# Kernel optimization log

Hardware: AMD Instinct MI355X
Metric: run time of the kernel (lower is better)

## Reference

```python
import jax, jax.numpy as jnp
import numpy as np


def setup_inputs() -> dict:
    key = jax.random.key(0)
    k1, k2, k3 = jax.random.split(key, 3)
    B, H, D, N = 2, 16, 64, 2048
    return {
        "query": jax.random.normal(k1, (B, H, D, N), dtype=jnp.float32),
        "key": jax.random.normal(k2, (B, H, D, N), dtype=jnp.float32),
        "value": jax.random.normal(k3, (B, H, D, N), dtype=jnp.float32),
    }


def reference(query, key, value):
    # NOTE: original torch code scales by sqrt(query.size(-1)) which,
    # given the [B,H,d,N] layout, is sqrt(N) (the sequence length), not sqrt(d).
    scale = query.shape[-1] ** 0.5
    # scores[b,h,q,k] = sum_d query[b,h,d,q] * key[b,h,d,k]
    scores = jnp.einsum("bhdq,bhdk->bhqk", query, key) / scale
    attn = jax.nn.softmax(scores, axis=-1)
    # out[b,h,q,v] = sum_k attn[b,h,q,k] * value[b,h,v,k]
    return jnp.einsum("bhqk,bhvk->bhqv", attn, value)
```

## Files before the change

### kernel.cpp

```cpp
#include <hip/hip_runtime.h>
#include <hip/hip_bf16.h>


typedef __attribute__((ext_vector_type(8))) short short8;
typedef __attribute__((ext_vector_type(4))) float f32x4;

#define NN 2048
#define DD 64

#if __has_builtin(__builtin_amdgcn_exp2f)
#define EXP2(x) __builtin_amdgcn_exp2f(x)
#else
#define EXP2(x) __expf(0.69314718056f * (x))
#endif

__device__ __forceinline__ unsigned pk2(float a, float b) {
  __hip_bfloat162 h = __float22bfloat162_rn(make_float2(a, b));
  unsigned u; __builtin_memcpy(&u, &h, 4); return u;
}
__device__ __forceinline__ short f2bf(float f) {
  union { float f; unsigned u; } x; x.f = f;
  unsigned r = (x.u + 0x7fffu + ((x.u >> 16) & 1u)) >> 16;
  return (short)r;
}

__global__ __launch_bounds__(256, 2) void attn_kernel(
    const float* __restrict__ Q, const float* __restrict__ K,
    const float* __restrict__ V, float* __restrict__ Out) {
  const int tid  = threadIdx.x;
  const int wave = tid >> 6, lane = tid & 63;
  const int quad = lane >> 4, l16 = lane & 15;
  const int sw   = l16 & 7;

  const int bh   = blockIdx.x >> 4;
  const int qblk = blockIdx.x & 15;

  const float* Qh = Q + (size_t)bh * DD * NN;
  const float* Kh = K + (size_t)bh * DD * NN;
  const float* Vh = V + (size_t)bh * DD * NN;
  float*       Oh = Out + (size_t)bh * NN * DD;

  __shared__ __align__(16) char ldsK[2][64 * 128];
  __shared__ __align__(16) char ldsV[2][64 * 128];
  __shared__ __align__(16) char ldsP[8][16 * 128];

  const float qscale = 0.031881407f;
  short8 bQ[2][2];
  int qb[2];
#pragma unroll
  for (int qt = 0; qt < 2; ++qt) {
    qb[qt] = qblk * 128 + (wave * 2 + qt) * 16;
#pragma unroll
    for (int h = 0; h < 2; ++h)
#pragma unroll
      for (int j = 0; j < 8; ++j) {
        int d = h * 32 + quad * 8 + j;
        bQ[qt][h][j] = f2bf(Qh[(size_t)d * NN + qb[qt] + l16] * qscale);
      }
  }

  f32x4 accO[2][4];
#pragma unroll
  for (int qt = 0; qt < 2; ++qt)
#pragma unroll
    for (int vt = 0; vt < 4; ++vt) accO[qt][vt] = (f32x4){0.f, 0.f, 0.f, 0.f};
  float lp[2] = {0.f, 0.f};

  const int da = tid & 15;
  const int kb4 = (tid >> 4) * 4;
  const int vv = tid >> 2;
  const int vko = (tid & 3) * 16;
  const float* kbase = Kh + (size_t)(da * 4) * NN + kb4;
  const float* vbase = Vh + (size_t)vv * NN + vko;
  char* Pq0 = ldsP[wave * 2];
  char* Pq1 = ldsP[wave * 2 + 1];

  float kreg[4][4];
  float4 vf0, vf1, vf2, vf3;
  auto load_kv = [&](int k0) {
#pragma unroll
    for (int i = 0; i < 4; ++i) {
      float4 t = *(const float4*)(kbase + (size_t)i * NN + k0);
      kreg[i][0] = t.x; kreg[i][1] = t.y; kreg[i][2] = t.z; kreg[i][3] = t.w;
    }
    const float4* pv = (const float4*)(vbase + k0);
    vf0 = pv[0]; vf1 = pv[1]; vf2 = pv[2]; vf3 = pv[3];
  };
  auto store_kv = [&](char* bK, char* bV) {
#pragma unroll
    for (int j = 0; j < 4; ++j) {
      int key = kb4 + j;
      int phys = (da >> 1) ^ (key & 7);
      uint2 w; w.x = pk2(kreg[0][j], kreg[1][j]); w.y = pk2(kreg[2][j], kreg[3][j]);
      *(uint2*)&bK[key * 128 + phys * 16 + (da & 1) * 8] = w;
    }
    int ph0 = ((vko >> 3)) ^ (vv & 7);
    int ph1 = ((vko >> 3) + 1) ^ (vv & 7);
    uint4 w0 = make_uint4(pk2(vf0.x, vf0.y), pk2(vf0.z, vf0.w),
                          pk2(vf1.x, vf1.y), pk2(vf1.z, vf1.w));
    uint4 w1 = make_uint4(pk2(vf2.x, vf2.y), pk2(vf2.z, vf2.w),
                          pk2(vf3.x, vf3.y), pk2(vf3.z, vf3.w));
    *(uint4*)&bV[vv * 128 + ph0 * 16] = w0;
    *(uint4*)&bV[vv * 128 + ph1 * 16] = w1;
  };

  load_kv(0);
  store_kv(ldsK[0], ldsV[0]);
  __syncthreads();

#pragma unroll 2
  for (int it = 0; it < 32; ++it) {
    const int cur = it & 1;
    load_kv(((it + 1) & 31) * 64);

    const char* cK = ldsK[cur];
    const char* cV = ldsV[cur];

    f32x4 s[2][4];
#pragma unroll
    for (int kt = 0; kt < 4; ++kt) {
      const int key = kt * 16 + l16;
      short8 aK0 = *(const short8*)&cK[key * 128 + ((quad)     ^ sw) * 16];
      short8 aK1 = *(const short8*)&cK[key * 128 + ((quad + 4) ^ sw) * 16];
      f32x4 z = (f32x4){0.f, 0.f, 0.f, 0.f};
      s[0][kt] = __builtin_amdgcn_mfma_f32_16x16x32_bf16(aK0, bQ[0][0], z, 0, 0, 0);
      s[0][kt] = __builtin_amdgcn_mfma_f32_16x16x32_bf16(aK1, bQ[0][1], s[0][kt], 0, 0, 0);
      s[1][kt] = __builtin_amdgcn_mfma_f32_16x16x32_bf16(aK0, bQ[1][0], z, 0, 0, 0);
      s[1][kt] = __builtin_amdgcn_mfma_f32_16x16x32_bf16(aK1, bQ[1][1], s[1][kt], 0, 0, 0);
    }

#pragma unroll
    for (int qt = 0; qt < 2; ++qt) {
      char* Pq = qt ? Pq1 : Pq0;
#pragma unroll
      for (int kt = 0; kt < 4; ++kt) {
        float p0 = EXP2(s[qt][kt][0]);
        float p1 = EXP2(s[qt][kt][1]);
        float p2 = EXP2(s[qt][kt][2]);
        float p3 = EXP2(s[qt][kt][3]);
        lp[qt] += (p0 + p1) + (p2 + p3);
        uint2 w; w.x = pk2(p0, p1); w.y = pk2(p2, p3);
        int phys = ((kt << 1) | (quad >> 1)) ^ sw;
        *(uint2*)&Pq[l16 * 128 + phys * 16 + (quad & 1) * 8] = w;
      }
    }

#pragma unroll
    for (int h2 = 0; h2 < 2; ++h2) {
      const int pg = (h2 * 4 + quad) ^ sw;
      short8 aP0 = *(const short8*)&Pq0[l16 * 128 + pg * 16];
      short8 aP1 = *(const short8*)&Pq1[l16 * 128 + pg * 16];
#pragma unroll
      for (int vt = 0; vt < 4; ++vt) {
        short8 bV = *(const short8*)&cV[(vt * 16 + l16) * 128 + pg * 16];
        accO[0][vt] = __builtin_amdgcn_mfma_f32_16x16x32_bf16(aP0, bV, accO[0][vt], 0, 0, 0);
        accO[1][vt] = __builtin_amdgcn_mfma_f32_16x16x32_bf16(aP1, bV, accO[1][vt], 0, 0, 0);
      }
    }

    store_kv(ldsK[cur ^ 1], ldsV[cur ^ 1]);
    __syncthreads();
  }

#pragma unroll
  for (int qt = 0; qt < 2; ++qt) {
    float l = lp[qt];
    l += __shfl_xor(l, 16, 64);
    l += __shfl_xor(l, 32, 64);
#pragma unroll
    for (int r = 0; r < 4; ++r) {
      float lr  = __shfl(l, quad * 4 + r, 64);
      float inv = 1.0f / lr;
      int q = qb[qt] + quad * 4 + r;
#pragma unroll
      for (int vt = 0; vt < 4; ++vt)
        Oh[(size_t)q * DD + vt * 16 + l16] = accO[qt][vt][r] * inv;
    }
  }
}

extern "C" void kernel_launch(void* const* d_in, const int* in_sizes, int n_in,
                              void* d_out, int out_size, void* d_ws, size_t ws_size,
                              hipStream_t stream) {
  const float* Q = (const float*)d_in[0];
  const float* K = (const float*)d_in[1];
  const float* V = (const float*)d_in[2];
  float* O = (float*)d_out;
  dim3 grid(2 * 16 * (NN / 128));
  attn_kernel<<<grid, dim3(256), 0, stream>>>(Q, K, V, O);
}
```

Measured before the change: 149.1 us.

## Halve queries per block, double grid, and map heads to XCDs

Each wave now handles one 16-query tile instead of two, so a block covers 64 queries and the grid doubles to 1024 blocks. Launch bounds allow 4 blocks per CU, and block indices are remapped so all blocks of a head land on the same XCD, aiming for better L2 reuse of K and V. The cost is that each block re-reads and converts the full K/V stream for half as much compute, doubling global K/V traffic and LDS staging work per query. It also drops the unroll pragma on the main loop.

After: 174.6 us. +17.1%, slower.

```diff
diff --git a/kernel.cpp b/kernel.cpp
--- a/kernel.cpp
+++ b/kernel.cpp
@@ -24,7 +24,7 @@
   return (short)r;
 }
 
-__global__ __launch_bounds__(256, 2) void attn_kernel(
+__global__ __launch_bounds__(256, 4) void attn_kernel(
     const float* __restrict__ Q, const float* __restrict__ K,
     const float* __restrict__ V, float* __restrict__ Out) {
   const int tid  = threadIdx.x;
@@ -32,8 +32,9 @@
   const int quad = lane >> 4, l16 = lane & 15;
   const int sw   = l16 & 7;
 
-  const int bh   = blockIdx.x >> 4;
-  const int qblk = blockIdx.x & 15;
+  const int xcd  = blockIdx.x & 7, slot = blockIdx.x >> 3;
+  const int bh   = xcd * 4 + (slot >> 5);
+  const int qblk = slot & 31;
 
   const float* Qh = Q + (size_t)bh * DD * NN;
   const float* Kh = K + (size_t)bh * DD * NN;
@@ -42,38 +43,31 @@
 
   __shared__ __align__(16) char ldsK[2][64 * 128];
   __shared__ __align__(16) char ldsV[2][64 * 128];
-  __shared__ __align__(16) char ldsP[8][16 * 128];
+  __shared__ __align__(16) char ldsP[4][16 * 128];
 
   const float qscale = 0.031881407f;
-  short8 bQ[2][2];
-  int qb[2];
+  const int q0 = qblk * 64 + wave * 16;
+  short8 bQ[2];
 #pragma unroll
-  for (int qt = 0; qt < 2; ++qt) {
-    qb[qt] = qblk * 128 + (wave * 2 + qt) * 16;
+  for (int h = 0; h < 2; ++h)
 #pragma unroll
-    for (int h = 0; h < 2; ++h)
+    for (int j = 0; j < 8; ++j) {
+      int d = h * 32 + quad * 8 + j;
+      bQ[h][j] = f2bf(Qh[(size_t)d * NN + q0 + l16] * qscale);
+    }
+
+  f32x4 accO[4];
 #pragma unroll
-      for (int j = 0; j < 8; ++j) {
-        int d = h * 32 + quad * 8 + j;
-        bQ[qt][h][j] = f2bf(Qh[(size_t)d * NN + qb[qt] + l16] * qscale);
-      }
-  }
+  for (int vt = 0; vt < 4; ++vt) accO[vt] = (f32x4){0.f, 0.f, 0.f, 0.f};
+  float lp = 0.f;
 
-  f32x4 accO[2][4];
-#pragma unroll
-  for (int qt = 0; qt < 2; ++qt)
-#pragma unroll
-    for (int vt = 0; vt < 4; ++vt) accO[qt][vt] = (f32x4){0.f, 0.f, 0.f, 0.f};
-  float lp[2] = {0.f, 0.f};
-
-  const int da = tid & 15;
+  const int da  = tid & 15;
   const int kb4 = (tid >> 4) * 4;
-  const int vv = tid >> 2;
+  const int vv  = tid >> 2;
   const int vko = (tid & 3) * 16;
   const float* kbase = Kh + (size_t)(da * 4) * NN + kb4;
   const float* vbase = Vh + (size_t)vv * NN + vko;
-  char* Pq0 = ldsP[wave * 2];
-  char* Pq1 = ldsP[wave * 2 + 1];
+  char* Pq = ldsP[wave];
 
   float kreg[4][4];
   float4 vf0, vf1, vf2, vf3;
@@ -94,7 +88,7 @@
       uint2 w; w.x = pk2(kreg[0][j], kreg[1][j]); w.y = pk2(kreg[2][j], kreg[3][j]);
       *(uint2*)&bK[key * 128 + phys * 16 + (da & 1) * 8] = w;
     }
-    int ph0 = ((vko >> 3)) ^ (vv & 7);
+    int ph0 = ((vko >> 3))     ^ (vv & 7);
     int ph1 = ((vko >> 3) + 1) ^ (vv & 7);
     uint4 w0 = make_uint4(pk2(vf0.x, vf0.y), pk2(vf0.z, vf0.w),
                           pk2(vf1.x, vf1.y), pk2(vf1.z, vf1.w));
@@ -108,7 +102,6 @@
   store_kv(ldsK[0], ldsV[0]);
   __syncthreads();
 
-#pragma unroll 2
   for (int it = 0; it < 32; ++it) {
     const int cur = it & 1;
     load_kv(((it + 1) & 31) * 64);
@@ -116,45 +109,37 @@
     const char* cK = ldsK[cur];
     const char* cV = ldsV[cur];
 
-    f32x4 s[2][4];
+    f32x4 s[4];
 #pragma unroll
     for (int kt = 0; kt < 4; ++kt) {
       const int key = kt * 16 + l16;
       short8 aK0 = *(const short8*)&cK[key * 128 + ((quad)     ^ sw) * 16];
       short8 aK1 = *(const short8*)&cK[key * 128 + ((quad + 4) ^ sw) * 16];
       f32x4 z = (f32x4){0.f, 0.f, 0.f, 0.f};
-      s[0][kt] = __builtin_amdgcn_mfma_f32_16x16x32_bf16(aK0, bQ[0][0], z, 0, 0, 0);
-      s[0][kt] = __builtin_amdgcn_mfma_f32_16x16x32_bf16(aK1, bQ[0][1], s[0][kt], 0, 0, 0);
-      s[1][kt] = __builtin_amdgcn_mfma_f32_16x16x32_bf16(aK0, bQ[1][0], z, 0, 0, 0);
-      s[1][kt] = __builtin_amdgcn_mfma_f32_16x16x32_bf16(aK1, bQ[1][1], s[1][kt], 0, 0, 0);
+      s[kt] = __builtin_amdgcn_mfma_f32_16x16x32_bf16(aK0, bQ[0], z, 0, 0, 0);
+      s[kt] = __builtin_amdgcn_mfma_f32_16x16x32_bf16(aK1, bQ[1], s[kt], 0, 0, 0);
     }
 
 #pragma unroll
-    for (int qt = 0; qt < 2; ++qt) {
-      char* Pq = qt ? Pq1 : Pq0;
-#pragma unroll
-      for (int kt = 0; kt < 4; ++kt) {
-        float p0 = EXP2(s[qt][kt][0]);
-        float p1 = EXP2(s[qt][kt][1]);
-        float p2 = EXP2(s[qt][kt][2]);
-        float p3 = EXP2(s[qt][kt][3]);
-        lp[qt] += (p0 + p1) + (p2 + p3);
-        uint2 w; w.x = pk2(p0, p1); w.y = pk2(p2, p3);
-        int phys = ((kt << 1) | (quad >> 1)) ^ sw;
-        *(uint2*)&Pq[l16 * 128 + phys * 16 + (quad & 1) * 8] = w;
-      }
+    for (int kt = 0; kt < 4; ++kt) {
+      float p0 = EXP2(s[kt][0]);
+      float p1 = EXP2(s[kt][1]);
+      float p2 = EXP2(s[kt][2]);
+      float p3 = EXP2(s[kt][3]);
+      lp += (p0 + p1) + (p2 + p3);
+      uint2 w; w.x = pk2(p0, p1); w.y = pk2(p2, p3);
+      int phys = ((kt << 1) | (quad >> 1)) ^ sw;
+      *(uint2*)&Pq[l16 * 128 + phys * 16 + (quad & 1) * 8] = w;
     }
 
 #pragma unroll
     for (int h2 = 0; h2 < 2; ++h2) {
       const int pg = (h2 * 4 + quad) ^ sw;
-      short8 aP0 = *(const short8*)&Pq0[l16 * 128 + pg * 16];
-      short8 aP1 = *(const short8*)&Pq1[l16 * 128 + pg * 16];
+      short8 aP = *(const short8*)&Pq[l16 * 128 + pg * 16];
 #pragma unroll
       for (int vt = 0; vt < 4; ++vt) {
         short8 bV = *(const short8*)&cV[(vt * 16 + l16) * 128 + pg * 16];
-        accO[0][vt] = __builtin_amdgcn_mfma_f32_16x16x32_bf16(aP0, bV, accO[0][vt], 0, 0, 0);
-        accO[1][vt] = __builtin_amdgcn_mfma_f32_16x16x32_bf16(aP1, bV, accO[1][vt], 0, 0, 0);
+        accO[vt] = __builtin_amdgcn_mfma_f32_16x16x32_bf16(aP, bV, accO[vt], 0, 0, 0);
       }
     }
 
@@ -162,20 +147,17 @@
     __syncthreads();
   }
 
+  float l = lp;
+  l += __shfl_xor(l, 16, 64);
+  l += __shfl_xor(l, 32, 64);
 #pragma unroll
-  for (int qt = 0; qt < 2; ++qt) {
-    float l = lp[qt];
-    l += __shfl_xor(l, 16, 64);
-    l += __shfl_xor(l, 32, 64);
+  for (int r = 0; r < 4; ++r) {
+    float lr  = __shfl(l, quad * 4 + r, 64);
+    float inv = 1.0f / lr;
+    int q = q0 + quad * 4 + r;
 #pragma unroll
-    for (int r = 0; r < 4; ++r) {
-      float lr  = __shfl(l, quad * 4 + r, 64);
-      float inv = 1.0f / lr;
-      int q = qb[qt] + quad * 4 + r;
-#pragma unroll
-      for (int vt = 0; vt < 4; ++vt)
-        Oh[(size_t)q * DD + vt * 16 + l16] = accO[qt][vt][r] * inv;
-    }
+    for (int vt = 0; vt < 4; ++vt)
+      Oh[(size_t)q * DD + vt * 16 + l16] = accO[vt][r] * inv;
   }
 }
 
@@ -186,6 +168,6 @@
   const float* K = (const float*)d_in[1];
   const float* V = (const float*)d_in[2];
   float* O = (float*)d_out;
-  dim3 grid(2 * 16 * (NN / 128));
+  dim3 grid(2 * 16 * (NN / 64));
   attn_kernel<<<grid, dim3(256), 0, stream>>>(Q, K, V, O);
 }
```
